# Optimization experiments

Measured on AMD Instinct MI355X. Metric: run time of the kernel, lower is better.

Reference implementation:

```python
import jax, jax.numpy as jnp
import numpy as np

H = 16      # num_heads
DH = 64     # dim_heads


def rotate_half(x):
    # '... (j d) -> ... j d', j=2; unbind -> (x1, x2); cat(-x2, x1)
    x1, x2 = jnp.split(x, 2, axis=-1)
    return jnp.concatenate([-x2, x1], axis=-1)


def apply_rope(t, freqs):
    # t: [b, h, s, d], freqs: [s, d] (rot_dim == d, so no unrotated tail)
    return t * jnp.cos(freqs) + rotate_half(t) * jnp.sin(freqs)


def setup_inputs() -> dict:
    key = jax.random.key(0)
    k1, k2, k3, k4 = jax.random.split(key, 4)
    B, S, D = 2, 2048, 1024
    x = jax.random.normal(k1, (B, S, D), dtype=jnp.float32)
    w_qkv = jax.random.normal(k2, (D, 3 * D), dtype=jnp.float32) * (D ** -0.5)
    w_out = jax.random.normal(k3, (D, D), dtype=jnp.float32) * (D ** -0.5)
    freqs = jax.random.normal(k4, (S, DH), dtype=jnp.float32)
    return {"x": x, "w_qkv": w_qkv, "w_out": w_out, "freqs": freqs}


def reference(x, w_qkv, w_out, freqs):
    B, S, D = x.shape
    qkv = x @ w_qkv                                   # [B, S, 3D]
    q, k, v = jnp.split(qkv, 3, axis=-1)
    def to_heads(t):
        return t.reshape(B, S, H, DH).transpose(0, 2, 1, 3)  # [B, H, S, DH]
    q, k, v = map(to_heads, (q, k, v))
    # rotary (computed in float32, which is already the working dtype)
    q = apply_rope(q, freqs)
    k = apply_rope(k, freqs)
    # causal SDPA, scale = 1/sqrt(dh)
    scale = DH ** -0.5
    scores = jnp.einsum('bhqd,bhkd->bhqk', q, k) * scale
    causal_mask = jnp.tril(jnp.ones((S, S), dtype=bool))
    scores = jnp.where(causal_mask, scores, jnp.finfo(scores.dtype).min)
    attn = jax.nn.softmax(scores, axis=-1)
    out = jnp.einsum('bhqk,bhkd->bhqd', attn, v)      # [B, H, S, DH]
    out = out.transpose(0, 2, 1, 3).reshape(B, S, D)  # 'b h n d -> b n (h d)'
    return out @ w_out
```

## Files before the change

kernel.cpp:

```cpp
#include <hip/hip_runtime.h>


typedef __bf16 bf16x8 __attribute__((ext_vector_type(8)));
typedef float f32x4 __attribute__((ext_vector_type(4)));

__device__ __forceinline__ unsigned short f2b(float f) {
  unsigned int u = __builtin_bit_cast(unsigned int, f);
  unsigned int lsb = (u >> 16) & 1u;
  u += 0x7fffu + lsb;
  return (unsigned short)(u >> 16);
}
__device__ __forceinline__ float b2f(unsigned short h) {
  unsigned int u = ((unsigned int)h) << 16;
  return __builtin_bit_cast(float, u);
}
__device__ __forceinline__ unsigned int pk2(float a, float b) {
  return (unsigned int)f2b(a) | ((unsigned int)f2b(b) << 16);
}
__device__ __forceinline__ unsigned int cvtpk(float lo, float hi) {
  unsigned int r;
  asm("v_cvt_pk_bf16_f32 %0, %1, %2" : "=v"(r) : "v"(lo), "v"(hi));
  return r;
}
__device__ __forceinline__ void gload16(const void* g, void* l) {
  __builtin_amdgcn_global_load_lds(
      (const __attribute__((address_space(1))) unsigned int*)g,
      (__attribute__((address_space(3))) unsigned int*)l, 16, 0, 0);
}

__global__ __launch_bounds__(256) void prologue_kernel(
    const float* __restrict__ x, unsigned short* __restrict__ xb,
    const float* __restrict__ freqs, float* __restrict__ cosT,
    float* __restrict__ sinT, const float* __restrict__ w_qkv,
    unsigned short* __restrict__ wqT, const float* __restrict__ w_out,
    unsigned short* __restrict__ woT) {
  __shared__ float tile[32][33];
  const int blk = blockIdx.x, tid = threadIdx.x;

  if (blk < 4096) {
    int i = (blk * 256 + tid) * 4;
    float4 v = *(const float4*)&x[i];
    ushort4 o;
    o.x = f2b(v.x); o.y = f2b(v.y); o.z = f2b(v.z); o.w = f2b(v.w);
    *(ushort4*)&xb[i] = o;
    return;
  }
  if (blk < 4608) {
    int i = (blk - 4096) * 256 + tid;
    float f = freqs[i];
    cosT[i] = cosf(f);
    sinT[i] = sinf(f);
    return;
  }
  const float* src;
  unsigned short* dst;
  int K, N, bx, by;
  if (blk < 7680) {
    src = w_qkv; dst = wqT; K = 1024; N = 3072;
    const int t = blk - 4608;
    bx = t % 96; by = t / 96;
  } else {
    src = w_out; dst = woT; K = 1024; N = 1024;
    const int t = blk - 7680;
    bx = t % 32; by = t / 32;
  }
  const int n0 = bx * 32, k0 = by * 32;
  const int c = tid & 31, r4 = tid >> 5;
#pragma unroll
  for (int p = 0; p < 4; ++p) {
    int r = r4 + p * 8;
    tile[r][c] = src[(size_t)(k0 + r) * N + n0 + c];
  }
  __syncthreads();
#pragma unroll
  for (int p = 0; p < 4; ++p) {
    int r = r4 + p * 8;
    dst[(size_t)(n0 + r) * K + k0 + c] = f2b(tile[c][r]);
  }
}

__global__ __launch_bounds__(512, 2) void gemm8(
    const unsigned short* __restrict__ A, const unsigned short* __restrict__ BT,
    unsigned short* __restrict__ Qb, unsigned short* __restrict__ Kbp,
    unsigned short* __restrict__ Vtg, const float* __restrict__ cosT,
    const float* __restrict__ sinT) {
  extern __shared__ unsigned short L[];
  const int K = 1024;
  const int tid = threadIdx.x, lane = tid & 63, w = tid >> 6;
  const int wr = w >> 2, wcn = w & 3;
  const int fr = lane & 15, oct = lane >> 4;

  const int raw = blockIdx.y * 12 + blockIdx.x;
  const int swz = (raw & 7) * 24 + (raw >> 3);
  const int m0 = (swz / 12) * 256, n0 = (swz % 12) * 256;

  const int sRow = tid >> 2;
  const int scol = ((tid & 3) ^ ((tid >> 3) & 3)) * 8;
  const int sOff = sRow * 32 + (tid & 3) * 8;
  const size_t aS0 = (size_t)(m0 + sRow) * K + scol;
  const size_t aS1 = (size_t)(m0 + 128 + sRow) * K + scol;
  const size_t bS0 = (size_t)(n0 + sRow) * K + scol;
  const size_t bS1 = (size_t)(n0 + 128 + sRow) * K + scol;

  const int pcx = (oct ^ ((fr >> 1) & 3)) * 8;

  f32x4 acc[8][4] = {};
  const int NT = 16;

#pragma unroll
  for (int kh = 0; kh < 2; ++kh) {
    const size_t gk = (size_t)kh * 32;
    gload16(&A[aS0 + gk], &L[kh * 8192 + sOff]);
    gload16(&A[aS1 + gk], &L[kh * 8192 + 4096 + sOff]);
    gload16(&BT[bS0 + gk], &L[16384 + kh * 8192 + sOff]);
    gload16(&BT[bS1 + gk], &L[16384 + kh * 8192 + 4096 + sOff]);
  }

  for (int t = 0; t < NT; ++t) {
    const int buf = t & 1, nbuf = buf ^ 1;
    const bool doStage = (t + 1 < NT);
#pragma unroll
    for (int kh = 0; kh < 2; ++kh) {
      if (t == NT - 1 && kh == 1) {
        asm volatile("s_waitcnt vmcnt(0)" ::: "memory");
      } else {
        asm volatile("s_waitcnt vmcnt(4)" ::: "memory");
      }
      __builtin_amdgcn_sched_barrier(0);
      __builtin_amdgcn_s_barrier();
      __builtin_amdgcn_sched_barrier(0);

      const unsigned short* Ab = &L[buf * 32768 + kh * 8192];
      const unsigned short* Bb = &L[buf * 32768 + 16384 + kh * 8192];

      bf16x8 af[8], bq[4];
#pragma unroll
      for (int i = 0; i < 8; ++i) {
        const int row = wr * 128 + i * 16 + fr;
        af[i] = __builtin_bit_cast(bf16x8, *(const uint4*)&Ab[row * 32 + pcx]);
      }
#pragma unroll
      for (int c = 0; c < 4; ++c) {
        const int brow = wcn * 64 + c * 16 + fr;
        bq[c] = __builtin_bit_cast(bf16x8, *(const uint4*)&Bb[brow * 32 + pcx]);
      }
      if (doStage) {
        const size_t gk = (size_t)(t + 1) * 64 + kh * 32;
        unsigned short* D = &L[nbuf * 32768 + kh * 8192];
        gload16(&A[aS0 + gk], &D[sOff]);
        gload16(&A[aS1 + gk], &D[4096 + sOff]);
        gload16(&BT[bS0 + gk], &D[16384 + sOff]);
        gload16(&BT[bS1 + gk], &D[16384 + 4096 + sOff]);
      }
      __builtin_amdgcn_s_setprio(1);
#pragma unroll
      for (int i = 0; i < 8; ++i)
#pragma unroll
        for (int c = 0; c < 4; ++c)
          acc[i][c] = __builtin_amdgcn_mfma_f32_16x16x32_bf16(af[i], bq[c], acc[i][c], 0, 0, 0);
      __builtin_amdgcn_s_setprio(0);
    }
  }

  const float QSCALE = 0.125f * 1.44269504f;
  const int part = n0 >> 10;
  const int hbase = (n0 & 1023) >> 6;
  if (part < 2) {
    unsigned short* dst = (part == 0) ? Qb : Kbp;
    const float scale = (part == 0) ? QSCALE : 1.0f;
    const int hh = hbase + wcn;
#pragma unroll
    for (int i = 0; i < 8; ++i)
#pragma unroll
      for (int r = 0; r < 4; ++r) {
        const int m = m0 + wr * 128 + i * 16 + oct * 4 + r;
        const int bb = m >> 11, s = m & 2047;
        const size_t ob = ((size_t)(bb * 16 + hh) * 2048 + s) * 64;
#pragma unroll
        for (int j = 0; j < 2; ++j) {
          const int d = j * 16 + fr;
          const float lo = acc[i][j][r], hi = acc[i][j + 2][r];
          const float cl = cosT[s * 64 + d], sl = sinT[s * 64 + d];
          const float ch = cosT[s * 64 + 32 + d], sh = sinT[s * 64 + 32 + d];
          dst[ob + d] = f2b((lo * cl - hi * sl) * scale);
          dst[ob + 32 + d] = f2b((hi * ch + lo * sh) * scale);
        }
      }
  } else {
#pragma unroll
    for (int p = 0; p < 2; ++p) {
      __syncthreads();
      if (wr == p) {
        unsigned short* vt = L + wcn * 8448;
#pragma unroll
        for (int i = 0; i < 8; ++i)
#pragma unroll
          for (int r = 0; r < 4; ++r) {
            const int row = i * 16 + oct * 4 + r;
#pragma unroll
            for (int j = 0; j < 4; ++j)
              vt[row * 66 + j * 16 + fr] = f2b(acc[i][j][r]);
          }
      }
      __syncthreads();
      const int sidx = tid >> 6, d = tid & 63;
      const int hd = sidx & 3, mgl = sidx >> 2;
      const unsigned short* tt = L + hd * 8448 + mgl * 64 * 66;
      const int mtile = m0 + (p * 2 + mgl) * 64;
      const int bb = mtile >> 11, sb = (mtile & 2047) >> 6;
      const int hv = hbase + hd;
      const size_t vb = (((size_t)(bb * 16 + hv) * 32 + sb) * 64 + d) * 64;
#pragma unroll
      for (int qq = 0; qq < 4; ++qq)
#pragma unroll
        for (int g = 0; g < 4; ++g) {
          ushort4 u;
          u.x = tt[(qq * 16 + g * 4 + 0) * 66 + d];
          u.y = tt[(qq * 16 + g * 4 + 1) * 66 + d];
          u.z = tt[(qq * 16 + g * 4 + 2) * 66 + d];
          u.w = tt[(qq * 16 + g * 4 + 3) * 66 + d];
          *(ushort4*)&Vtg[vb + (qq >> 1) * 32 + g * 8 + (qq & 1) * 4] = u;
        }
    }
  }
}

__global__ __launch_bounds__(256, 2) void gemm2_ring(const unsigned short* __restrict__ A,
                                                     const unsigned short* __restrict__ BT,
                                                     float* __restrict__ C,
                                                     int M, int N, int K) {
  extern __shared__ unsigned short L[];
  const int tid = threadIdx.x, lane = tid & 63, w = tid >> 6;
  const int wr = w >> 1, wc = w & 1;
  const int fr = lane & 15, oct = lane >> 4;
  const int m0 = blockIdx.y * 128, n0 = blockIdx.x * 64;

  const int sr = tid >> 2;
  const int scol = ((tid & 3) ^ ((tid >> 3) & 3)) * 8;
  const size_t aR0 = (size_t)(m0 + sr) * K + scol;
  const size_t aR1 = (size_t)(m0 + 64 + sr) * K + scol;
  const size_t bR0 = (size_t)(n0 + sr) * K + scol;

  f32x4 acc[4][2] = {};
  const int T = K >> 5;

  for (int pt = 0; pt < 3; ++pt) {
    unsigned short* Ln = &L[pt * 6144];
    const size_t gk = (size_t)pt * 32;
    gload16(&A[aR0 + gk], &Ln[tid * 8]);
    gload16(&A[aR1 + gk], &Ln[2048 + tid * 8]);
    gload16(&BT[bR0 + gk], &Ln[4096 + tid * 8]);
  }

  for (int t = 0; t < T; ++t) {
    if (t + 3 <= T) {
      asm volatile("s_waitcnt vmcnt(6)" ::: "memory");
    } else if (t + 2 == T) {
      asm volatile("s_waitcnt vmcnt(3)" ::: "memory");
    } else {
      asm volatile("s_waitcnt vmcnt(0)" ::: "memory");
    }
    __builtin_amdgcn_sched_barrier(0);
    __builtin_amdgcn_s_barrier();
    __builtin_amdgcn_sched_barrier(0);

    const unsigned short* Lb = &L[(t & 3) * 6144];
    unsigned short* Ln = &L[((t + 3) & 3) * 6144];
    const size_t gk = (size_t)(t + 3) * 32;
    const bool doStage = (t + 3 < T);

    bf16x8 af[4], bq[2];
#pragma unroll
    for (int i = 0; i < 4; ++i) {
      const int ra = wr * 64 + i * 16 + fr;
      af[i] = __builtin_bit_cast(
          bf16x8, *(const uint4*)&Lb[ra * 32 + ((oct ^ ((ra >> 1) & 3)) * 8)]);
    }
#pragma unroll
    for (int j = 0; j < 2; ++j) {
      const int rb = wc * 32 + j * 16 + fr;
      bq[j] = __builtin_bit_cast(
          bf16x8,
          *(const uint4*)&Lb[4096 + rb * 32 + ((oct ^ ((rb >> 1) & 3)) * 8)]);
    }
    if (doStage) {
      gload16(&A[aR0 + gk], &Ln[tid * 8]);
      gload16(&A[aR1 + gk], &Ln[2048 + tid * 8]);
      gload16(&BT[bR0 + gk], &Ln[4096 + tid * 8]);
    }
    __builtin_amdgcn_s_setprio(1);
#pragma unroll
    for (int i = 0; i < 4; ++i)
#pragma unroll
      for (int j = 0; j < 2; ++j)
        acc[i][j] = __builtin_amdgcn_mfma_f32_16x16x32_bf16(af[i], bq[j], acc[i][j], 0, 0, 0);
    __builtin_amdgcn_s_setprio(0);
  }

#pragma unroll
  for (int i = 0; i < 4; ++i)
#pragma unroll
    for (int j = 0; j < 2; ++j)
#pragma unroll
      for (int r = 0; r < 4; ++r)
        C[(size_t)(m0 + wr * 64 + i * 16 + oct * 4 + r) * N + n0 + wc * 32 +
          j * 16 + fr] = acc[i][j][r];
}

__global__ __launch_bounds__(512, 4) void attn_mfma(const unsigned short* __restrict__ Qb,
                                                    const unsigned short* __restrict__ Kb,
                                                    const unsigned short* __restrict__ Vtg,
                                                    unsigned short* __restrict__ attnb) {
  extern __shared__ unsigned short KV[];
  const int bid = blockIdx.x + 16 * (blockIdx.y + 16 * blockIdx.z);
  const int xcd = bid & 7, slot = bid >> 3;
  const int qt0 = slot & 15;
  const int gq = xcd + 8 * (slot >> 4);
  const int h = gq & 15, b = gq >> 4;
  const int qt1 = 31 - qt0;
  const int tid = threadIdx.x, lane = tid & 63, w = tid >> 6;
  const int fr = lane & 15, oct = lane >> 4;
  const int grp = w >> 2, wq = w & 3;
  const int nhA = 16 - qt0, nhB = 15 - qt0;

  const size_t bh = (size_t)(b * 16 + h);
  const unsigned short* Kbase = Kb + bh * 131072;
  const unsigned short* Vbase = Vtg + bh * 131072;

  const int qtP1 = grp ? qt1 : qt0;
  const unsigned short* Qp1 = Qb + (bh * 2048 + qtP1 * 64 + wq * 16 + fr) * 64;
  const bf16x8 qa0 = __builtin_bit_cast(bf16x8, *(const uint4*)(Qp1 + oct * 8));
  const bf16x8 qa1 = __builtin_bit_cast(bf16x8, *(const uint4*)(Qp1 + 32 + oct * 8));
  const unsigned short* Qp2 = Qb + (bh * 2048 + qt1 * 64 + wq * 16 + fr) * 64;
  const bf16x8 qb0 = __builtin_bit_cast(bf16x8, *(const uint4*)(Qp2 + oct * 8));
  const bf16x8 qb1 = __builtin_bit_cast(bf16x8, *(const uint4*)(Qp2 + 32 + oct * 8));

  const int frx = fr & 7;
  const int rc0 = (oct ^ frx) * 8;
  const int rc1 = ((4 + oct) ^ frx) * 8;

  float m_prev = -1e30f;
  f32x4 acc[4] = {};
  f32x4 accl = {};

  uint4 onesu;
  onesu.x = 0x3F803F80u; onesu.y = 0x3F803F80u;
  onesu.z = 0x3F803F80u; onesu.w = 0x3F803F80u;
  const bf16x8 onesf = __builtin_bit_cast(bf16x8, onesu);

  auto tile_step = [&](int buf, bf16x8 q0, bf16x8 q1, bool domask) {
    const unsigned short* Kbuf = &KV[buf * 4096];
    const unsigned short* Vbuf = &KV[(4 + buf) * 4096];
    f32x4 s4[4];
    __builtin_amdgcn_s_setprio(1);
#pragma unroll
    for (int t = 0; t < 4; ++t) {
      bf16x8 kf0 = __builtin_bit_cast(bf16x8, *(const uint4*)&Kbuf[(t * 16 + fr) * 64 + rc0]);
      bf16x8 kf1 = __builtin_bit_cast(bf16x8, *(const uint4*)&Kbuf[(t * 16 + fr) * 64 + rc1]);
      f32x4 s = {};
      s = __builtin_amdgcn_mfma_f32_16x16x32_bf16(kf0, q0, s, 0, 0, 0);
      s = __builtin_amdgcn_mfma_f32_16x16x32_bf16(kf1, q1, s, 0, 0, 0);
      s4[t] = s;
    }
    __builtin_amdgcn_s_setprio(0);
    if (domask) {
#pragma unroll
      for (int t = 0; t < 4; ++t)
#pragma unroll
        for (int r = 0; r < 4; ++r)
          if (t * 16 + oct * 4 + r > wq * 16 + fr) s4[t][r] = -1e30f;
    }

    float pm = -1e30f;
#pragma unroll
    for (int t = 0; t < 4; ++t)
#pragma unroll
      for (int r = 0; r < 4; ++r) pm = fmaxf(pm, s4[t][r]);
    const bool need = __any(pm - m_prev > 11.0f);
    if (need) {
      float pmf = fmaxf(pm, __shfl_xor(pm, 16));
      pmf = fmaxf(pmf, __shfl_xor(pmf, 32));
      float mnew = fmaxf(m_prev, pmf);
      float cf = __builtin_amdgcn_exp2f(m_prev - mnew);
      m_prev = mnew;
      float cfr[4];
#pragma unroll
      for (int r = 0; r < 4; ++r) cfr[r] = __shfl(cf, oct * 4 + r);
#pragma unroll
      for (int t2 = 0; t2 < 4; ++t2)
#pragma unroll
        for (int r = 0; r < 4; ++r) acc[t2][r] *= cfr[r];
#pragma unroll
      for (int r = 0; r < 4; ++r) accl[r] *= cfr[r];
    }
    const float mc = m_prev;
#pragma unroll
    for (int t = 0; t < 4; ++t)
#pragma unroll
      for (int r = 0; r < 4; ++r)
        s4[t][r] = __builtin_amdgcn_exp2f(s4[t][r] - mc);

    uint4 pw0, pw1;
    pw0.x = cvtpk(s4[0][0], s4[0][1]); pw0.y = cvtpk(s4[0][2], s4[0][3]);
    pw0.z = cvtpk(s4[1][0], s4[1][1]); pw0.w = cvtpk(s4[1][2], s4[1][3]);
    pw1.x = cvtpk(s4[2][0], s4[2][1]); pw1.y = cvtpk(s4[2][2], s4[2][3]);
    pw1.z = cvtpk(s4[3][0], s4[3][1]); pw1.w = cvtpk(s4[3][2], s4[3][3]);
    const bf16x8 pa0 = __builtin_bit_cast(bf16x8, pw0);
    const bf16x8 pa1 = __builtin_bit_cast(bf16x8, pw1);

    __builtin_amdgcn_s_setprio(1);
#pragma unroll
    for (int t2 = 0; t2 < 4; ++t2) {
      bf16x8 vf0 = __builtin_bit_cast(bf16x8, *(const uint4*)&Vbuf[(t2 * 16 + fr) * 64 + rc0]);
      bf16x8 vf1 = __builtin_bit_cast(bf16x8, *(const uint4*)&Vbuf[(t2 * 16 + fr) * 64 + rc1]);
      f32x4 a = acc[t2];
      a = __builtin_amdgcn_mfma_f32_16x16x32_bf16(pa0, vf0, a, 0, 0, 0);
      a = __builtin_amdgcn_mfma_f32_16x16x32_bf16(pa1, vf1, a, 0, 0, 0);
      acc[t2] = a;
    }
    {
      f32x4 a = accl;
      a = __builtin_amdgcn_mfma_f32_16x16x32_bf16(pa0, onesf, a, 0, 0, 0);
      a = __builtin_amdgcn_mfma_f32_16x16x32_bf16(pa1, onesf, a, 0, 0, 0);
      accl = a;
    }
    __builtin_amdgcn_s_setprio(0);
  };

  auto write_out = [&](int qtile) {
#pragma unroll
    for (int r = 0; r < 4; ++r) {
      float linv = 1.f / accl[r];
      size_t orow = (size_t)(b * 2048 + qtile * 64 + wq * 16 + oct * 4 + r);
#pragma unroll
      for (int t2 = 0; t2 < 4; ++t2)
        attnb[orow * 1024 + h * 64 + t2 * 16 + fr] = f2b(acc[t2][r] * linv);
    }
  };

  const int srow = tid >> 3, lc1 = tid & 7;
  const int soff = srow * 64 + (lc1 ^ (srow & 7)) * 8;
  const unsigned short* kp1 = Kbase + srow * 64 + lc1 * 8;
  const unsigned short* vp1 = Vbase + srow * 64 + lc1 * 8;
  {
    uint4 kr = *(const uint4*)kp1;
    uint4 vr = *(const uint4*)vp1;
    *(uint4*)&KV[0 * 4096 + soff] = kr;
    *(uint4*)&KV[4 * 4096 + soff] = vr;
  }
  __syncthreads();

  for (int kb = 0; kb <= qt0; ++kb) {
    uint4 kr = *(const uint4*)(kp1 + (size_t)(kb + 1) * 4096);
    uint4 vr = *(const uint4*)(vp1 + (size_t)(kb + 1) * 4096);
    uint4 kr2, vr2;
    const bool extra = (kb == qt0) && (nhB > 0);
    if (extra) {
      kr2 = *(const uint4*)(kp1 + (size_t)17 * 4096);
      vr2 = *(const uint4*)(vp1 + (size_t)17 * 4096);
    }
    tile_step(kb & 1, qa0, qa1, kb == qtP1);
    const int nb = (kb + 1) & 1;
    *(uint4*)&KV[nb * 4096 + soff] = kr;
    *(uint4*)&KV[(4 + nb) * 4096 + soff] = vr;
    if (extra) {
      *(uint4*)&KV[2 * 4096 + soff] = kr2;
      *(uint4*)&KV[6 * 4096 + soff] = vr2;
    }
    __syncthreads();
  }

  if (grp == 0) {
    write_out(qt0);
    m_prev = -1e30f;
    f32x4 zz = {};
    accl = zz;
#pragma unroll
    for (int t2 = 0; t2 < 4; ++t2) acc[t2] = zz;
  }

  const int t2id = tid & 255;
  const int sk2 = t2id >> 2, lq = t2id & 3;
  const int lcA = lq * 2, lcB = lq * 2 + 1;
  const int ofA = sk2 * 64 + (lcA ^ (sk2 & 7)) * 8;
  const int ofB = sk2 * 64 + (lcB ^ (sk2 & 7)) * 8;
  const int sc2 = lq * 16;
  const int cnt = grp ? nhB : nhA;
  for (int i = 0; i < nhA; ++i) {
    const int kbm = grp ? (17 + i) : (qt0 + 1 + i);
    const int buf = grp ? (2 + (i & 1)) : (kbm & 1);
    uint4 k0, k1, v0, v1;
    const bool pf = (i + 1 < cnt);
    if (pf) {
      const unsigned short* ks = Kbase + (size_t)((kbm + 1) * 64 + sk2) * 64 + sc2;
      const unsigned short* vs = Vbase + (size_t)((kbm + 1) * 64 + sk2) * 64 + sc2;
      k0 = *(const uint4*)ks; k1 = *(const uint4*)(ks + 8);
      v0 = *(const uint4*)vs; v1 = *(const uint4*)(vs + 8);
    }
    if (i < cnt) tile_step(buf, qb0, qb1, kbm == qt1);
    if (pf) {
      const int nb = grp ? (2 + ((i + 1) & 1)) : ((kbm + 1) & 1);
      *(uint4*)&KV[nb * 4096 + ofA] = k0;
      *(uint4*)&KV[nb * 4096 + ofB] = k1;
      *(uint4*)&KV[(4 + nb) * 4096 + ofA] = v0;
      *(uint4*)&KV[(4 + nb) * 4096 + ofB] = v1;
    }
    __syncthreads();
  }

  float* MF = (float*)KV;
  if (grp == 1) {
#pragma unroll
    for (int t2 = 0; t2 < 4; ++t2)
#pragma unroll
      for (int r = 0; r < 4; ++r)
        MF[(wq * 16 + oct * 4 + r) * 68 + t2 * 16 + fr] = acc[t2][r];
    if (fr == 0) {
#pragma unroll
      for (int r = 0; r < 4; ++r) MF[4352 + wq * 16 + oct * 4 + r] = accl[r];
    }
    if (oct == 0) MF[4416 + wq * 16 + fr] = m_prev;
  }
  __syncthreads();
  if (grp == 0) {
    float mB = MF[4416 + wq * 16 + fr];
    float mS = fmaxf(m_prev, mB);
    float fA = __builtin_amdgcn_exp2f(m_prev - mS);
    float fB = __builtin_amdgcn_exp2f(mB - mS);
    float fAr[4], fBr[4];
#pragma unroll
    for (int r = 0; r < 4; ++r) {
      fAr[r] = __shfl(fA, oct * 4 + r);
      fBr[r] = __shfl(fB, oct * 4 + r);
    }
#pragma unroll
    for (int r = 0; r < 4; ++r)
      accl[r] = accl[r] * fAr[r] + MF[4352 + wq * 16 + oct * 4 + r] * fBr[r];
#pragma unroll
    for (int t2 = 0; t2 < 4; ++t2)
#pragma unroll
      for (int r = 0; r < 4; ++r)
        acc[t2][r] = acc[t2][r] * fAr[r] +
                     MF[(wq * 16 + oct * 4 + r) * 68 + t2 * 16 + fr] * fBr[r];
    write_out(qt1);
  }
}

extern "C" void kernel_launch(void* const* d_in, const int* in_sizes, int n_in,
                              void* d_out, int out_size, void* d_ws, size_t ws_size,
                              hipStream_t stream) {
  const float* x     = (const float*)d_in[0];
  const float* w_qkv = (const float*)d_in[1];
  const float* w_out = (const float*)d_in[2];
  const float* freqs = (const float*)d_in[3];
  float* out = (float*)d_out;

  char* ws = (char*)d_ws;
  unsigned short* Qb   = (unsigned short*)(ws + 25165824);
  unsigned short* Kb   = (unsigned short*)(ws + 33554432);
  unsigned short* Vtg  = (unsigned short*)(ws + 41943040);
  unsigned short* attnb= (unsigned short*)(ws + 50331648);
  unsigned short* wqT  = (unsigned short*)(ws + 58720256);
  unsigned short* woT  = (unsigned short*)(ws + 65011712);
  unsigned short* xb   = (unsigned short*)(ws + 67108864);
  float* cosT          = (float*)(ws + 75497472);
  float* sinT          = (float*)(ws + 76021760);

  (void)hipFuncSetAttribute((const void*)gemm8,
                            hipFuncAttributeMaxDynamicSharedMemorySize, 131072);
  (void)hipFuncSetAttribute((const void*)gemm2_ring,
                            hipFuncAttributeMaxDynamicSharedMemorySize, 49152);
  (void)hipFuncSetAttribute((const void*)attn_mfma,
                            hipFuncAttributeMaxDynamicSharedMemorySize, 65536);

  prologue_kernel<<<8704, 256, 0, stream>>>(x, xb, freqs, cosT, sinT, w_qkv,
                                            wqT, w_out, woT);
  gemm8<<<dim3(12, 16), 512, 131072, stream>>>(xb, wqT, Qb, Kb, Vtg, cosT,
                                               sinT);
  attn_mfma<<<dim3(16, 16, 2), 512, 65536, stream>>>(Qb, Kb, Vtg, attnb);
  gemm2_ring<<<dim3(16, 32), 256, 49152, stream>>>(attnb, woT, out, 4096, 1024, 1024);
}
```

Baseline: 91.58 us.

## Use four-stage LDS ring pipeline with split A loads in QKV GEMM

The QKV projection GEMM mainloop moves from a double-buffered 64-wide K step to a 4-slot ring of 32-wide K tiles, with three tiles in flight. It also splits the global loads and MFMA work into two halves per step so copies interleave with compute. The wave-to-tile mapping changes so each wave reads B from a different sub-block. This aims to hide memory latency better, at the cost of more barriers per K and a changed accumulator-to-output mapping that the unchanged epilogue may no longer match.

Result: no change. 93.05 us (+1.6%).

```diff
diff --git a/kernel.cpp b/kernel.cpp
--- a/kernel.cpp
+++ b/kernel.cpp
@@ -89,6 +89,7 @@
   const int tid = threadIdx.x, lane = tid & 63, w = tid >> 6;
   const int wr = w >> 2, wcn = w & 3;
   const int fr = lane & 15, oct = lane >> 4;
+  const int bhalf = wcn >> 1, bb0 = (wcn & 1) * 64;
 
   const int raw = blockIdx.y * 12 + blockIdx.x;
   const int swz = (raw & 7) * 24 + (raw >> 3);
@@ -105,61 +106,77 @@
   const int pcx = (oct ^ ((fr >> 1) & 3)) * 8;
 
   f32x4 acc[8][4] = {};
-  const int NT = 16;
-
-#pragma unroll
-  for (int kh = 0; kh < 2; ++kh) {
-    const size_t gk = (size_t)kh * 32;
-    gload16(&A[aS0 + gk], &L[kh * 8192 + sOff]);
-    gload16(&A[aS1 + gk], &L[kh * 8192 + 4096 + sOff]);
-    gload16(&BT[bS0 + gk], &L[16384 + kh * 8192 + sOff]);
-    gload16(&BT[bS1 + gk], &L[16384 + kh * 8192 + 4096 + sOff]);
-  }
-
-  for (int t = 0; t < NT; ++t) {
-    const int buf = t & 1, nbuf = buf ^ 1;
-    const bool doStage = (t + 1 < NT);
-#pragma unroll
-    for (int kh = 0; kh < 2; ++kh) {
-      if (t == NT - 1 && kh == 1) {
-        asm volatile("s_waitcnt vmcnt(0)" ::: "memory");
-      } else {
-        asm volatile("s_waitcnt vmcnt(4)" ::: "memory");
-      }
-      __builtin_amdgcn_sched_barrier(0);
-      __builtin_amdgcn_s_barrier();
-      __builtin_amdgcn_sched_barrier(0);
-
-      const unsigned short* Ab = &L[buf * 32768 + kh * 8192];
-      const unsigned short* Bb = &L[buf * 32768 + 16384 + kh * 8192];
-
-      bf16x8 af[8], bq[4];
-#pragma unroll
-      for (int i = 0; i < 8; ++i) {
-        const int row = wr * 128 + i * 16 + fr;
-        af[i] = __builtin_bit_cast(bf16x8, *(const uint4*)&Ab[row * 32 + pcx]);
-      }
-#pragma unroll
-      for (int c = 0; c < 4; ++c) {
-        const int brow = wcn * 64 + c * 16 + fr;
-        bq[c] = __builtin_bit_cast(bf16x8, *(const uint4*)&Bb[brow * 32 + pcx]);
-      }
-      if (doStage) {
-        const size_t gk = (size_t)(t + 1) * 64 + kh * 32;
-        unsigned short* D = &L[nbuf * 32768 + kh * 8192];
-        gload16(&A[aS0 + gk], &D[sOff]);
-        gload16(&A[aS1 + gk], &D[4096 + sOff]);
-        gload16(&BT[bS0 + gk], &D[16384 + sOff]);
-        gload16(&BT[bS1 + gk], &D[16384 + 4096 + sOff]);
-      }
-      __builtin_amdgcn_s_setprio(1);
-#pragma unroll
-      for (int i = 0; i < 8; ++i)
-#pragma unroll
-        for (int c = 0; c < 4; ++c)
-          acc[i][c] = __builtin_amdgcn_mfma_f32_16x16x32_bf16(af[i], bq[c], acc[i][c], 0, 0, 0);
-      __builtin_amdgcn_s_setprio(0);
-    }
+  const int T = K >> 5;
+
+  for (int pt = 0; pt < 3; ++pt) {
+    unsigned short* Ln = &L[pt * 16384];
+    const size_t gk = (size_t)pt * 32;
+    gload16(&A[aS0 + gk], &Ln[sOff]);
+    gload16(&A[aS1 + gk], &Ln[4096 + sOff]);
+    gload16(&BT[bS0 + gk], &Ln[8192 + sOff]);
+    gload16(&BT[bS1 + gk], &Ln[12288 + sOff]);
+  }
+
+  for (int t = 0; t < T; ++t) {
+    if (t + 3 <= T) {
+      asm volatile("s_waitcnt vmcnt(8)" ::: "memory");
+    } else if (t + 2 == T) {
+      asm volatile("s_waitcnt vmcnt(4)" ::: "memory");
+    } else {
+      asm volatile("s_waitcnt vmcnt(0)" ::: "memory");
+    }
+    __builtin_amdgcn_sched_barrier(0);
+    __builtin_amdgcn_s_barrier();
+    __builtin_amdgcn_sched_barrier(0);
+
+    const unsigned short* Lb = &L[(t & 3) * 16384];
+    unsigned short* Ln = &L[((t + 3) & 3) * 16384];
+    const size_t gk = (size_t)(t + 3) * 32;
+    const bool doStage = (t + 3 < T);
+
+    bf16x8 afr[4], bfr[4];
+#pragma unroll
+    for (int j = 0; j < 4; ++j) {
+      const int rb = bb0 + j * 16 + fr;
+      bfr[j] = __builtin_bit_cast(
+          bf16x8, *(const uint4*)&Lb[8192 + bhalf * 4096 + rb * 32 + pcx]);
+    }
+#pragma unroll
+    for (int i = 0; i < 4; ++i) {
+      const int ra = i * 16 + fr;
+      afr[i] = __builtin_bit_cast(
+          bf16x8, *(const uint4*)&Lb[wr * 4096 + ra * 32 + pcx]);
+    }
+    if (doStage) {
+      gload16(&A[aS0 + gk], &Ln[sOff]);
+      gload16(&BT[bS0 + gk], &Ln[8192 + sOff]);
+    }
+    __builtin_amdgcn_s_setprio(1);
+#pragma unroll
+    for (int i = 0; i < 4; ++i)
+#pragma unroll
+      for (int j = 0; j < 4; ++j)
+        acc[i][j] = __builtin_amdgcn_mfma_f32_16x16x32_bf16(afr[i], bfr[j], acc[i][j], 0, 0, 0);
+    __builtin_amdgcn_s_setprio(0);
+
+#pragma unroll
+    for (int i = 0; i < 4; ++i) {
+      const int ra = 64 + i * 16 + fr;
+      afr[i] = __builtin_bit_cast(
+          bf16x8, *(const uint4*)&Lb[wr * 4096 + ra * 32 + pcx]);
+    }
+    if (doStage) {
+      gload16(&A[aS1 + gk], &Ln[4096 + sOff]);
+      gload16(&BT[bS1 + gk], &Ln[12288 + sOff]);
+    }
+    __builtin_amdgcn_s_setprio(1);
+#pragma unroll
+    for (int i = 0; i < 4; ++i)
+#pragma unroll
+      for (int j = 0; j < 4; ++j)
+        acc[4 + i][j] =
+            __builtin_amdgcn_mfma_f32_16x16x32_bf16(afr[i], bfr[j], acc[4 + i][j], 0, 0, 0);
+    __builtin_amdgcn_s_setprio(0);
   }
 
   const float QSCALE = 0.125f * 1.44269504f;
```
